# Performance work log

Hardware: AMD Instinct MI355X
Metric: run time of the kernel (lower is better)

## Reference

```python
import jax, jax.numpy as jnp
import numpy as np

N_HEADS = 16

def setup_inputs() -> dict:
    key = jax.random.key(0)
    ks = jax.random.split(key, 9)
    B, S, E = 2, 2048, 1024
    s = 1.0 / np.sqrt(E)
    return {
        "x":  jax.random.normal(ks[0], (B, S, E), jnp.float32),
        "Wq": jax.random.normal(ks[1], (E, E), jnp.float32) * s,
        "bq": jax.random.normal(ks[2], (E,), jnp.float32) * 0.01,
        "Wk": jax.random.normal(ks[3], (E, E), jnp.float32) * s,
        "bk": jax.random.normal(ks[4], (E,), jnp.float32) * 0.01,
        "Wv": jax.random.normal(ks[5], (E, E), jnp.float32) * s,
        "bv": jax.random.normal(ks[6], (E,), jnp.float32) * 0.01,
        "Wo": jax.random.normal(ks[7], (E, E), jnp.float32) * s,
        "bo": jax.random.normal(ks[8], (E,), jnp.float32) * 0.01,
    }

def reference(x, Wq, bq, Wk, bk, Wv, bv, Wo, bo):
    B, S, E = x.shape
    H = N_HEADS
    D = E // H
    # torch nn.Linear: y = x @ W.T + b
    q = (x @ Wq.T + bq).reshape(B, S, H, D)
    k = (x @ Wk.T + bk).reshape(B, S, H, D)
    v = (x @ Wv.T + bv).reshape(B, S, H, D)
    # scores: [B, H, Q, K]
    scores = jnp.einsum('bqnd,bknd->bnqk', q, k) / jnp.sqrt(jnp.float32(D))
    # NOTE: original code softmaxes over dim=1 == the HEADS axis (faithful quirk)
    attn = jax.nn.softmax(scores, axis=1)
    # dropout p=0 -> identity
    out = jnp.einsum('bnqk,bknd->bnqd', attn, v)      # [B, H, Q, D]
    out = out.transpose(0, 2, 1, 3).reshape(B, S, E)  # [B, S, E]
    return out @ Wo.T + bo
```

## Files before the change

kernel.cpp:

```cpp
#include <hip/hip_runtime.h>
#include <cstddef>
#include <cstdint>

#define BATCH 2
#define S_LEN 2048
#define E_DIM 1024
#define NH    16
#define HD    64
#define M_ROWS (BATCH * S_LEN)

#define QSCALE 0.18033688011112042f

typedef unsigned short u16;
typedef short     bf16x8 __attribute__((ext_vector_type(8)));
typedef _Float16  f16x8  __attribute__((ext_vector_type(8)));
typedef __fp16    h16x2  __attribute__((ext_vector_type(2)));
typedef float     f32x4  __attribute__((ext_vector_type(4)));

__device__ __forceinline__ u16 f2bf(float f) {
    union { float f; unsigned u; } v; v.f = f;
    unsigned r = v.u + 0x7fffu + ((v.u >> 16) & 1u);
    return (u16)(r >> 16);
}
__device__ __forceinline__ float bf2f(u16 h) {
    union { unsigned u; float f; } v; v.u = ((unsigned)h) << 16;
    return v.f;
}

__device__ __forceinline__ void load_lds16(const u16* g, u16* l) {
    __builtin_amdgcn_global_load_lds(
        (const __attribute__((address_space(1))) unsigned int*)g,
        (__attribute__((address_space(3))) unsigned int*)l, 16, 0, 0);
}

__global__ void cvt_bf16(const float* __restrict__ in, u16* __restrict__ out, int n)
{
    int i = (blockIdx.x * 256 + threadIdx.x) * 4;
    if (i + 3 < n) {
        float4 v = *(const float4*)(in + i);
        u16 o[4] = { f2bf(v.x), f2bf(v.y), f2bf(v.z), f2bf(v.w) };
        *(uint2*)(out + i) = *(const uint2*)o;
    }
}

__global__ void cvt_w3(const float* __restrict__ Wq, const float* __restrict__ Wk,
                       const float* __restrict__ Wv, u16* __restrict__ out)
{
    const int seg = blockIdx.y;
    const float* src = (seg == 0) ? Wq : (seg == 1) ? Wk : Wv;
    int i = (blockIdx.x * 256 + threadIdx.x) * 4;
    float4 v = *(const float4*)(src + i);
    u16 o[4] = { f2bf(v.x), f2bf(v.y), f2bf(v.z), f2bf(v.w) };
    *(uint2*)(out + (size_t)seg * E_DIM * E_DIM + i) = *(const uint2*)o;
}

__global__ void combine_ctx(const u16* __restrict__ a, const u16* __restrict__ b,
                            u16* __restrict__ c, int n)
{
    int i = (blockIdx.x * 256 + threadIdx.x) * 4;
    if (i + 3 < n) {
        uint2 ua = *(const uint2*)(a + i);
        uint2 ub = *(const uint2*)(b + i);
        const u16* pa = (const u16*)&ua; const u16* pb = (const u16*)&ub;
        u16 o[4];
#pragma unroll
        for (int j = 0; j < 4; ++j) o[j] = f2bf(bf2f(pa[j]) + bf2f(pb[j]));
        *(uint2*)(c + i) = *(const uint2*)o;
    }
}

__global__ __launch_bounds__(256)
void gemm_qkv(const u16* __restrict__ A, const u16* __restrict__ W3,
              const float* __restrict__ bq, const float* __restrict__ bk,
              const float* __restrict__ bv,
              u16* __restrict__ Qb, u16* __restrict__ Kb, u16* __restrict__ Vtb)
{
    __shared__ u16 Al[128 * 32];
    __shared__ u16 Bl[128 * 32];
    const int K = E_DIM;
    const int t = threadIdx.x;
    const int w = t >> 6, lane = t & 63;
    const int quad = lane >> 4, lm = lane & 15;
    const int wy = w >> 1, wx = w & 1;
    const int m0 = blockIdx.x * 128, n0 = blockIdx.y * 128;
    const int lrow  = lane >> 2;
    const int lcol8 = (lane & 3) * 8;

    f32x4 acc[4][4] = {};

    for (int kb = 0; kb < K; kb += 32) {
        __syncthreads();
#pragma unroll
        for (int i = 0; i < 2; ++i) {
            const int r0 = w * 32 + i * 16;
            load_lds16(A  + (size_t)(m0 + r0 + lrow) * K + kb + lcol8, &Al[r0 * 32]);
            load_lds16(W3 + (size_t)(n0 + r0 + lrow) * K + kb + lcol8, &Bl[r0 * 32]);
        }
        __syncthreads();

        bf16x8 af[4], bfr[4];
#pragma unroll
        for (int i = 0; i < 4; ++i)
            af[i] = *(const bf16x8*)(Al + (wy * 64 + i * 16 + lm) * 32 + quad * 8);
#pragma unroll
        for (int j = 0; j < 4; ++j)
            bfr[j] = *(const bf16x8*)(Bl + (wx * 64 + j * 16 + lm) * 32 + quad * 8);
#pragma unroll
        for (int i = 0; i < 4; ++i)
#pragma unroll
            for (int j = 0; j < 4; ++j)
                acc[i][j] = __builtin_amdgcn_mfma_f32_16x16x32_bf16(af[i], bfr[j], acc[i][j], 0, 0, 0);
    }

    const int seg = n0 >> 10;
    const int nl0 = n0 & 1023;
    const float* bs = (seg == 0) ? bq : (seg == 1) ? bk : bv;

    if (seg < 2) {
        u16* dst = (seg == 0) ? Qb : Kb;
        const float scl = (seg == 0) ? QSCALE : 1.0f;
#pragma unroll
        for (int j = 0; j < 4; ++j) {
            const int n = nl0 + wx * 64 + j * 16 + lm;
            const float bias = bs[n];
#pragma unroll
            for (int i = 0; i < 4; ++i) {
                const int mrow = m0 + wy * 64 + i * 16 + quad * 4;
#pragma unroll
                for (int rg = 0; rg < 4; ++rg)
                    dst[(size_t)(mrow + rg) * E_DIM + n] = f2bf((acc[i][j][rg] + bias) * scl);
            }
        }
    } else {
#pragma unroll
        for (int j = 0; j < 4; ++j) {
            const int n = nl0 + wx * 64 + j * 16 + lm;
            const float bias = bs[n];
#pragma unroll
            for (int i = 0; i < 4; ++i) {
                const int mrow = m0 + wy * 64 + i * 16 + quad * 4;
                const int batch = mrow >> 11;
                const int sloc  = mrow & 2047;
                u16 o[4];
#pragma unroll
                for (int rg = 0; rg < 4; ++rg) {
                    union { _Float16 h; u16 u; } cv;
                    cv.h = (_Float16)(acc[i][j][rg] + bias);
                    o[rg] = cv.u;
                }
                *(uint2*)&Vtb[(size_t)batch * E_DIM * S_LEN + (size_t)n * S_LEN + sloc]
                    = *(const uint2*)o;
            }
        }
    }
}

__global__ __launch_bounds__(256)
void gemm_wo(const u16* __restrict__ A, const u16* __restrict__ B,
             const float* __restrict__ bias, float* __restrict__ C)
{
    __shared__ u16 Al[128 * 32];
    __shared__ u16 Bl[128 * 32];
    const int K = E_DIM, N = E_DIM;
    const int t = threadIdx.x;
    const int w = t >> 6, lane = t & 63;
    const int quad = lane >> 4, lm = lane & 15;
    const int wy = w >> 1, wx = w & 1;
    const int m0 = blockIdx.x * 128, n0 = blockIdx.y * 128;
    const int lrow  = lane >> 2;
    const int lcol8 = (lane & 3) * 8;

    f32x4 acc[4][4] = {};

    for (int kb = 0; kb < K; kb += 32) {
        __syncthreads();
#pragma unroll
        for (int i = 0; i < 2; ++i) {
            const int r0 = w * 32 + i * 16;
            load_lds16(A + (size_t)(m0 + r0 + lrow) * K + kb + lcol8, &Al[r0 * 32]);
            load_lds16(B + (size_t)(n0 + r0 + lrow) * K + kb + lcol8, &Bl[r0 * 32]);
        }
        __syncthreads();

        bf16x8 af[4], bfr[4];
#pragma unroll
        for (int i = 0; i < 4; ++i)
            af[i] = *(const bf16x8*)(Al + (wy * 64 + i * 16 + lm) * 32 + quad * 8);
#pragma unroll
        for (int j = 0; j < 4; ++j)
            bfr[j] = *(const bf16x8*)(Bl + (wx * 64 + j * 16 + lm) * 32 + quad * 8);
#pragma unroll
        for (int i = 0; i < 4; ++i)
#pragma unroll
            for (int j = 0; j < 4; ++j)
                acc[i][j] = __builtin_amdgcn_mfma_f32_16x16x32_bf16(af[i], bfr[j], acc[i][j], 0, 0, 0);
    }

#pragma unroll
    for (int j = 0; j < 4; ++j) {
        const int n = n0 + wx * 64 + j * 16 + lm;
        const float bs = bias[n];
#pragma unroll
        for (int i = 0; i < 4; ++i) {
            const int mrow = m0 + wy * 64 + i * 16 + quad * 4;
#pragma unroll
            for (int rg = 0; rg < 4; ++rg)
                C[(size_t)(mrow + rg) * N + n] = acc[i][j][rg] + bs;
        }
    }
}

#define QKT_ST(S4W, KOFF)                                                     \
  _Pragma("unroll")                                                           \
  for (int kt = 0; kt < 2; ++kt) {                                            \
    f32x4 sacc_[2][2];                                                        \
    _Pragma("unroll")                                                         \
    for (int hp = 0; hp < 2; ++hp) {                                          \
      bf16x8 kf0_ = *(const bf16x8*)(K + kmat                                 \
                    + (size_t)((KOFF) + kt * 16 + lm) * E_DIM                 \
                    + (h0 + hp) * 64 + quad * 8);                             \
      bf16x8 kf1_ = *(const bf16x8*)(K + kmat                                 \
                    + (size_t)((KOFF) + kt * 16 + lm) * E_DIM                 \
                    + (h0 + hp) * 64 + 32 + quad * 8);                        \
      _Pragma("unroll")                                                       \
      for (int s = 0; s < 2; ++s) {                                           \
        f32x4 sf_ = {};                                                       \
        sf_ = __builtin_amdgcn_mfma_f32_16x16x32_bf16(kf0_, qf[s][hp][0], sf_, 0, 0, 0); \
        sf_ = __builtin_amdgcn_mfma_f32_16x16x32_bf16(kf1_, qf[s][hp][1], sf_, 0, 0, 0); \
        sacc_[hp][s] = sf_;                                                   \
      }                                                                       \
    }                                                                         \
    _Pragma("unroll")                                                         \
    for (int s = 0; s < 2; ++s)                                               \
      _Pragma("unroll")                                                       \
      for (int rg = 0; rg < 4; ++rg) {                                        \
        union { h16x2 v; unsigned u; } pk_;                                   \
        pk_.v = __builtin_amdgcn_cvt_pkrtz(sacc_[0][s][rg], sacc_[1][s][rg]); \
        const int kl_  = kt * 16 + quad * 4 + rg;                             \
        const int qph_ = ((s * 16 + lm) + 8 * quad) & 31;                     \
        *(unsigned*)((S4W) + (size_t)(kl_ * 32 + qph_) * 18 + 2 * w) = pk_.u; \
      }                                                                       \
  }

#define SM_ST(S4R, P5W)                                                       \
  {                                                                           \
    float pv0[16], pv1[16];                                                   \
    _Pragma("unroll")                                                         \
    for (int e = 0; e < 2; ++e) {                                             \
      const int kk_ = 2 * sj + e;                                             \
      const u16* base_ = (S4R) + (size_t)(kk_ * 32 + qrot) * 18;              \
      union { uint4 u; __fp16 hh[8]; } r0_, r1_;                              \
      r0_.u = *(const uint4*)(base_);                                         \
      r1_.u = *(const uint4*)(base_ + 8);                                     \
      float s_[16];                                                           \
      _Pragma("unroll")                                                       \
      for (int z = 0; z < 8; ++z) {                                           \
        s_[z] = (float)r0_.hh[z]; s_[8 + z] = (float)r1_.hh[z];               \
      }                                                                       \
      const float m_ =                                                        \
          fmaxf(fmaxf(fmaxf(fmaxf(s_[0], s_[1]), fmaxf(s_[2], s_[3])),        \
                      fmaxf(fmaxf(s_[4], s_[5]), fmaxf(s_[6], s_[7]))),       \
                fmaxf(fmaxf(fmaxf(s_[8], s_[9]), fmaxf(s_[10], s_[11])),      \
                      fmaxf(fmaxf(s_[12], s_[13]), fmaxf(s_[14], s_[15])))); \
      _Pragma("unroll")                                                       \
      for (int hh = 0; hh < 16; ++hh)                                         \
        s_[hh] = __builtin_amdgcn_exp2f(s_[hh] - m_);                         \
      const float sum_ =                                                      \
          (((s_[0] + s_[1]) + (s_[2] + s_[3])) + ((s_[4] + s_[5]) + (s_[6] + s_[7]))) + \
          (((s_[8] + s_[9]) + (s_[10] + s_[11])) + ((s_[12] + s_[13]) + (s_[14] + s_[15]))); \
      const float inv_ = __builtin_amdgcn_rcpf(sum_);                         \
      if (e == 0) {                                                           \
        _Pragma("unroll")                                                     \
        for (int hh = 0; hh < 16; ++hh) pv0[hh] = s_[hh] * inv_;              \
      } else {                                                                \
        _Pragma("unroll")                                                     \
        for (int hh = 0; hh < 16; ++hh) pv1[hh] = s_[hh] * inv_;              \
      }                                                                       \
    }                                                                         \
    _Pragma("unroll")                                                         \
    for (int hh = 0; hh < 16; ++hh) {                                         \
      union { h16x2 v; unsigned u; } cv_;                                     \
      cv_.v = __builtin_amdgcn_cvt_pkrtz(pv0[hh], pv1[hh]);                   \
      *(unsigned*)((P5W) + (size_t)hh * 1280 + sq * 40 + 2 * sj) = cv_.u;     \
    }                                                                         \
  }

#define V_ST(KOFF)                                                            \
  _Pragma("unroll")                                                           \
  for (int hp = 0; hp < 2; ++hp)                                              \
    _Pragma("unroll")                                                         \
    for (int dt = 0; dt < 4; ++dt)                                            \
      vf[hp][dt] = *(const f16x8*)(Vt + vtb                                   \
                   + (size_t)((h0 + hp) * 64 + dt * 16 + lm) * S_LEN          \
                   + (KOFF) + quad * 8);

#define PV_ST(P5R)                                                            \
  _Pragma("unroll")                                                           \
  for (int hp = 0; hp < 2; ++hp)                                              \
    _Pragma("unroll")                                                         \
    for (int s = 0; s < 2; ++s) {                                             \
      f16x8 pa_ = *(const f16x8*)((P5R) + (size_t)(h0 + hp) * 1280            \
                                  + (s * 16 + lm) * 40 + quad * 8);           \
      _Pragma("unroll")                                                       \
      for (int dt = 0; dt < 4; ++dt)                                          \
        oacc[hp][s][dt] = __builtin_amdgcn_mfma_f32_16x16x32_f16(             \
                              pa_, vf[hp][dt], oacc[hp][s][dt], 0, 0, 0);     \
    }

#define PHASE_END                                                             \
  asm volatile("s_waitcnt lgkmcnt(0)" ::: "memory");                          \
  __builtin_amdgcn_s_barrier();

__global__ __launch_bounds__(512, 2)
void attn_v16(const u16* __restrict__ Q, const u16* __restrict__ K,
              const u16* __restrict__ Vt, u16* __restrict__ ctxA,
              u16* __restrict__ ctxB)
{
    __shared__ __align__(16) u16 smem[77824];

    const int t     = threadIdx.x;
    const int w     = t >> 6;
    const int lane  = t & 63;
    const int quad  = lane >> 4, lm = lane & 15;

    const int i     = blockIdx.x;
    const int xcd   = i & 7;
    const int combo = xcd >> 1;
    const int b     = combo >> 1;
    const int khalf = combo & 1;
    const int slot  = i >> 3;
    const int qt    = ((xcd & 1) << 5) | slot;
    const int q0    = qt * 32;

    const size_t qbase = ((size_t)b * S_LEN + q0) * E_DIM;
    const size_t kmat  = (size_t)b * S_LEN * E_DIM;
    const size_t vtb   = (size_t)b * E_DIM * S_LEN;

    const int h0 = 2 * w;

    bf16x8 qf[2][2][2];
#pragma unroll
    for (int s = 0; s < 2; ++s)
#pragma unroll
        for (int hp = 0; hp < 2; ++hp)
#pragma unroll
            for (int hf = 0; hf < 2; ++hf)
                qf[s][hp][hf] = *(const bf16x8*)(Q + qbase
                                + (size_t)(s * 16 + lm) * E_DIM
                                + (h0 + hp) * 64 + hf * 32 + quad * 8);

    f32x4 oacc[2][2][4] = {};
    f16x8 vf[2][4];
    const int kbeg = khalf * (S_LEN / 2);
    const int sq = t & 31, sj = t >> 5;
    const int qrot = (sq + 8 * ((sj >> 1) & 3)) & 31;

    u16* const S4_0 = smem;
    u16* const S4_1 = smem + 18432;
    u16* const P5_0 = smem + 36864;
    u16* const P5_1 = smem + 57344;

    QKT_ST(S4_0, kbeg)
    PHASE_END
    QKT_ST(S4_1, kbeg + 32)
    SM_ST (S4_0, P5_0)
    PHASE_END

    for (int c = 2; c < 32; ++c) {
        u16* S4w = (c & 1) ? S4_1 : S4_0;
        u16* S4r = (c & 1) ? S4_0 : S4_1;
        u16* P5w = (c & 1) ? P5_0 : P5_1;
        u16* P5r = (c & 1) ? P5_1 : P5_0;
        V_ST  (kbeg + (c - 2) * 32)
        QKT_ST(S4w, kbeg + c * 32)
        SM_ST (S4r, P5w)
        PV_ST (P5r)
        PHASE_END
    }

    V_ST  (kbeg + 30 * 32)
    SM_ST (S4_1, P5_1)
    PV_ST (P5_0)
    PHASE_END
    V_ST  (kbeg + 31 * 32)
    PV_ST (P5_1)

    __syncthreads();
    u16* Ol = smem;
#pragma unroll
    for (int hp = 0; hp < 2; ++hp) {
        const int h = h0 + hp;
#pragma unroll
        for (int s = 0; s < 2; ++s)
#pragma unroll
            for (int dt = 0; dt < 4; ++dt)
#pragma unroll
                for (int rg = 0; rg < 4; ++rg)
                    Ol[(size_t)(s * 16 + quad * 4 + rg) * 1024 + h * 64 + dt * 16 + lm]
                        = f2bf(oacc[hp][s][dt][rg]);
    }
    __syncthreads();
    u16* dst = khalf ? ctxB : ctxA;
#pragma unroll
    for (int i2 = 0; i2 < 8; ++i2) {
        const int unit = i2 * 512 + t;
        const int r = unit >> 7, cu = unit & 127;
        *(bf16x8*)(dst + ((size_t)b * S_LEN + q0 + r) * E_DIM + cu * 8) =
            *(const bf16x8*)(Ol + (size_t)r * 1024 + cu * 8);
    }
}

#undef QKT_ST
#undef SM_ST
#undef V_ST
#undef PV_ST
#undef PHASE_END

extern "C" void kernel_launch(void* const* d_in, const int* in_sizes, int n_in,
                              void* d_out, int out_size, void* d_ws, size_t ws_size,
                              hipStream_t stream)
{
    const float* x  = (const float*)d_in[0];
    const float* Wq = (const float*)d_in[1];
    const float* bq = (const float*)d_in[2];
    const float* Wk = (const float*)d_in[3];
    const float* bk = (const float*)d_in[4];
    const float* Wv = (const float*)d_in[5];
    const float* bv = (const float*)d_in[6];
    const float* Wo = (const float*)d_in[7];
    const float* bo = (const float*)d_in[8];
    float* out = (float*)d_out;

    const size_t MAT = (size_t)M_ROWS * E_DIM;
    const size_t WSZ = (size_t)E_DIM * E_DIM;
    u16* xb   = (u16*)d_ws;
    u16* W3   = xb   + MAT;
    u16* Wob  = W3   + 3 * WSZ;
    u16* Qb   = Wob  + WSZ;
    u16* Kb   = Qb   + MAT;
    u16* Vtb  = Kb   + MAT;
    u16* ctxA = Vtb  + MAT;
    u16* ctxB = ctxA + MAT;

    cvt_bf16<<<(int)(MAT / 1024), 256, 0, stream>>>(x, xb, (int)MAT);
    dim3 wgrid(WSZ / 1024, 3);
    cvt_w3<<<wgrid, 256, 0, stream>>>(Wq, Wk, Wv, W3);
    cvt_bf16<<<(int)(WSZ / 1024), 256, 0, stream>>>(Wo, Wob, (int)WSZ);

    dim3 qkvgrid(M_ROWS / 128, 3 * E_DIM / 128);
    gemm_qkv<<<qkvgrid, 256, 0, stream>>>(xb, W3, bq, bk, bv, Qb, Kb, Vtb);

    attn_v16<<<BATCH * 64 * 2, 512, 0, stream>>>(Qb, Kb, Vtb, ctxA, ctxB);

    combine_ctx<<<(int)(MAT / 1024), 256, 0, stream>>>(ctxA, ctxB, xb, (int)MAT);

    dim3 ogrid(M_ROWS / 128, E_DIM / 128);
    gemm_wo<<<ogrid, 256, 0, stream>>>(xb, Wob, bo, out);
}
```

Before: 298.0 us.

## Double K-tile in GEMMs with XOR-swizzled LDS and register-prefetch K in attention

Both projection GEMMs now stage a 64-wide K slice per iteration instead of 32, halving the number of barrier pairs, and XOR-swizzle the LDS column groups so the fragment reads avoid bank conflicts. The attention kernel splits the K-fragment global loads out of the QK^T stage and loads the next chunk's K fragments into a second register set one phase ahead, with the main loop unrolled by two to ping-pong between them. This hides global load latency for K behind the softmax and PV work. The cost is doubled LDS per GEMM block and extra registers in the attention kernel, which runs under a launch bound of two blocks per unit and may spill.

```diff
diff --git a/kernel.cpp b/kernel.cpp
--- a/kernel.cpp
+++ b/kernel.cpp
@@ -75,41 +75,50 @@
               const float* __restrict__ bv,
               u16* __restrict__ Qb, u16* __restrict__ Kb, u16* __restrict__ Vtb)
 {
-    __shared__ u16 Al[128 * 32];
-    __shared__ u16 Bl[128 * 32];
+    __shared__ u16 Al[128 * 64];
+    __shared__ u16 Bl[128 * 64];
     const int K = E_DIM;
     const int t = threadIdx.x;
     const int w = t >> 6, lane = t & 63;
     const int quad = lane >> 4, lm = lane & 15;
     const int wy = w >> 1, wx = w & 1;
     const int m0 = blockIdx.x * 128, n0 = blockIdx.y * 128;
-    const int lrow  = lane >> 2;
-    const int lcol8 = (lane & 3) * 8;
+    const int lrow   = lane >> 3;
+    const int lcolsw = ((lane & 7) ^ lrow) * 8;
 
     f32x4 acc[4][4] = {};
 
-    for (int kb = 0; kb < K; kb += 32) {
+    for (int kb = 0; kb < K; kb += 64) {
         __syncthreads();
 #pragma unroll
-        for (int i = 0; i < 2; ++i) {
-            const int r0 = w * 32 + i * 16;
-            load_lds16(A  + (size_t)(m0 + r0 + lrow) * K + kb + lcol8, &Al[r0 * 32]);
-            load_lds16(W3 + (size_t)(n0 + r0 + lrow) * K + kb + lcol8, &Bl[r0 * 32]);
+        for (int i = 0; i < 4; ++i) {
+            const int r0 = w * 32 + i * 8;
+            load_lds16(A  + (size_t)(m0 + r0 + lrow) * K + kb + lcolsw, &Al[r0 * 64]);
+            load_lds16(W3 + (size_t)(n0 + r0 + lrow) * K + kb + lcolsw, &Bl[r0 * 64]);
         }
         __syncthreads();
 
-        bf16x8 af[4], bfr[4];
-#pragma unroll
-        for (int i = 0; i < 4; ++i)
-            af[i] = *(const bf16x8*)(Al + (wy * 64 + i * 16 + lm) * 32 + quad * 8);
-#pragma unroll
-        for (int j = 0; j < 4; ++j)
-            bfr[j] = *(const bf16x8*)(Bl + (wx * 64 + j * 16 + lm) * 32 + quad * 8);
-#pragma unroll
-        for (int i = 0; i < 4; ++i)
-#pragma unroll
-            for (int j = 0; j < 4; ++j)
-                acc[i][j] = __builtin_amdgcn_mfma_f32_16x16x32_bf16(af[i], bfr[j], acc[i][j], 0, 0, 0);
+#pragma unroll
+        for (int kk = 0; kk < 2; ++kk) {
+            bf16x8 af[4], bfr[4];
+#pragma unroll
+            for (int i = 0; i < 4; ++i) {
+                const int rr = wy * 64 + i * 16 + lm;
+                const int pg = (kk * 4 + quad) ^ (rr & 7);
+                af[i] = *(const bf16x8*)(Al + rr * 64 + pg * 8);
+            }
+#pragma unroll
+            for (int j = 0; j < 4; ++j) {
+                const int rr = wx * 64 + j * 16 + lm;
+                const int pg = (kk * 4 + quad) ^ (rr & 7);
+                bfr[j] = *(const bf16x8*)(Bl + rr * 64 + pg * 8);
+            }
+#pragma unroll
+            for (int i = 0; i < 4; ++i)
+#pragma unroll
+                for (int j = 0; j < 4; ++j)
+                    acc[i][j] = __builtin_amdgcn_mfma_f32_16x16x32_bf16(af[i], bfr[j], acc[i][j], 0, 0, 0);
+        }
     }
 
     const int seg = n0 >> 10;
@@ -159,41 +168,50 @@
 void gemm_wo(const u16* __restrict__ A, const u16* __restrict__ B,
              const float* __restrict__ bias, float* __restrict__ C)
 {
-    __shared__ u16 Al[128 * 32];
-    __shared__ u16 Bl[128 * 32];
+    __shared__ u16 Al[128 * 64];
+    __shared__ u16 Bl[128 * 64];
     const int K = E_DIM, N = E_DIM;
     const int t = threadIdx.x;
     const int w = t >> 6, lane = t & 63;
     const int quad = lane >> 4, lm = lane & 15;
     const int wy = w >> 1, wx = w & 1;
     const int m0 = blockIdx.x * 128, n0 = blockIdx.y * 128;
-    const int lrow  = lane >> 2;
-    const int lcol8 = (lane & 3) * 8;
+    const int lrow   = lane >> 3;
+    const int lcolsw = ((lane & 7) ^ lrow) * 8;
 
     f32x4 acc[4][4] = {};
 
-    for (int kb = 0; kb < K; kb += 32) {
+    for (int kb = 0; kb < K; kb += 64) {
         __syncthreads();
 #pragma unroll
-        for (int i = 0; i < 2; ++i) {
-            const int r0 = w * 32 + i * 16;
-            load_lds16(A + (size_t)(m0 + r0 + lrow) * K + kb + lcol8, &Al[r0 * 32]);
-            load_lds16(B + (size_t)(n0 + r0 + lrow) * K + kb + lcol8, &Bl[r0 * 32]);
+        for (int i = 0; i < 4; ++i) {
+            const int r0 = w * 32 + i * 8;
+            load_lds16(A + (size_t)(m0 + r0 + lrow) * K + kb + lcolsw, &Al[r0 * 64]);
+            load_lds16(B + (size_t)(n0 + r0 + lrow) * K + kb + lcolsw, &Bl[r0 * 64]);
         }
         __syncthreads();
 
-        bf16x8 af[4], bfr[4];
-#pragma unroll
-        for (int i = 0; i < 4; ++i)
-            af[i] = *(const bf16x8*)(Al + (wy * 64 + i * 16 + lm) * 32 + quad * 8);
-#pragma unroll
-        for (int j = 0; j < 4; ++j)
-            bfr[j] = *(const bf16x8*)(Bl + (wx * 64 + j * 16 + lm) * 32 + quad * 8);
-#pragma unroll
-        for (int i = 0; i < 4; ++i)
-#pragma unroll
-            for (int j = 0; j < 4; ++j)
-                acc[i][j] = __builtin_amdgcn_mfma_f32_16x16x32_bf16(af[i], bfr[j], acc[i][j], 0, 0, 0);
+#pragma unroll
+        for (int kk = 0; kk < 2; ++kk) {
+            bf16x8 af[4], bfr[4];
+#pragma unroll
+            for (int i = 0; i < 4; ++i) {
+                const int rr = wy * 64 + i * 16 + lm;
+                const int pg = (kk * 4 + quad) ^ (rr & 7);
+                af[i] = *(const bf16x8*)(Al + rr * 64 + pg * 8);
+            }
+#pragma unroll
+            for (int j = 0; j < 4; ++j) {
+                const int rr = wx * 64 + j * 16 + lm;
+                const int pg = (kk * 4 + quad) ^ (rr & 7);
+                bfr[j] = *(const bf16x8*)(Bl + rr * 64 + pg * 8);
+            }
+#pragma unroll
+            for (int i = 0; i < 4; ++i)
+#pragma unroll
+                for (int j = 0; j < 4; ++j)
+                    acc[i][j] = __builtin_amdgcn_mfma_f32_16x16x32_bf16(af[i], bfr[j], acc[i][j], 0, 0, 0);
+        }
     }
 
 #pragma unroll
@@ -210,26 +228,32 @@
     }
 }
 
-#define QKT_ST(S4W, KOFF)                                                     \
+#define KLOAD(KX, KOFF)                                                       \
+  _Pragma("unroll")                                                           \
+  for (int kt = 0; kt < 2; ++kt)                                              \
+    _Pragma("unroll")                                                         \
+    for (int hp = 0; hp < 2; ++hp) {                                          \
+      KX[kt][hp][0] = *(const bf16x8*)(K + kmat                               \
+                      + (size_t)((KOFF) + kt * 16 + lm) * E_DIM               \
+                      + (h0 + hp) * 64 + quad * 8);                           \
+      KX[kt][hp][1] = *(const bf16x8*)(K + kmat                               \
+                      + (size_t)((KOFF) + kt * 16 + lm) * E_DIM               \
+                      + (h0 + hp) * 64 + 32 + quad * 8);                      \
+    }
+
+#define QKT_R(KX, S4W)                                                        \
   _Pragma("unroll")                                                           \
   for (int kt = 0; kt < 2; ++kt) {                                            \
     f32x4 sacc_[2][2];                                                        \
     _Pragma("unroll")                                                         \
-    for (int hp = 0; hp < 2; ++hp) {                                          \
-      bf16x8 kf0_ = *(const bf16x8*)(K + kmat                                 \
-                    + (size_t)((KOFF) + kt * 16 + lm) * E_DIM                 \
-                    + (h0 + hp) * 64 + quad * 8);                             \
-      bf16x8 kf1_ = *(const bf16x8*)(K + kmat                                 \
-                    + (size_t)((KOFF) + kt * 16 + lm) * E_DIM                 \
-                    + (h0 + hp) * 64 + 32 + quad * 8);                        \
+    for (int hp = 0; hp < 2; ++hp)                                            \
       _Pragma("unroll")                                                       \
       for (int s = 0; s < 2; ++s) {                                           \
         f32x4 sf_ = {};                                                       \
-        sf_ = __builtin_amdgcn_mfma_f32_16x16x32_bf16(kf0_, qf[s][hp][0], sf_, 0, 0, 0); \
-        sf_ = __builtin_amdgcn_mfma_f32_16x16x32_bf16(kf1_, qf[s][hp][1], sf_, 0, 0, 0); \
+        sf_ = __builtin_amdgcn_mfma_f32_16x16x32_bf16(KX[kt][hp][0], qf[s][hp][0], sf_, 0, 0, 0); \
+        sf_ = __builtin_amdgcn_mfma_f32_16x16x32_bf16(KX[kt][hp][1], qf[s][hp][1], sf_, 0, 0, 0); \
         sacc_[hp][s] = sf_;                                                   \
       }                                                                       \
-    }                                                                         \
     _Pragma("unroll")                                                         \
     for (int s = 0; s < 2; ++s)                                               \
       _Pragma("unroll")                                                       \
@@ -312,7 +336,7 @@
   __builtin_amdgcn_s_barrier();
 
 __global__ __launch_bounds__(512, 2)
-void attn_v16(const u16* __restrict__ Q, const u16* __restrict__ K,
+void attn_v17(const u16* __restrict__ Q, const u16* __restrict__ K,
               const u16* __restrict__ Vt, u16* __restrict__ ctxA,
               u16* __restrict__ ctxB)
 {
@@ -351,6 +375,7 @@
 
     f32x4 oacc[2][2][4] = {};
     f16x8 vf[2][4];
+    bf16x8 kA[2][2][2], kB[2][2][2];
     const int kbeg = khalf * (S_LEN / 2);
     const int sq = t & 31, sj = t >> 5;
     const int qrot = (sq + 8 * ((sj >> 1) & 3)) & 31;
@@ -360,21 +385,29 @@
     u16* const P5_0 = smem + 36864;
     u16* const P5_1 = smem + 57344;
 
-    QKT_ST(S4_0, kbeg)
+    KLOAD(kA, kbeg)
+    QKT_R (kA, S4_0)
+    KLOAD (kB, kbeg + 32)
     PHASE_END
-    QKT_ST(S4_1, kbeg + 32)
+    QKT_R (kB, S4_1)
+    KLOAD (kA, kbeg + 64)
     SM_ST (S4_0, P5_0)
     PHASE_END
 
-    for (int c = 2; c < 32; ++c) {
-        u16* S4w = (c & 1) ? S4_1 : S4_0;
-        u16* S4r = (c & 1) ? S4_0 : S4_1;
-        u16* P5w = (c & 1) ? P5_0 : P5_1;
-        u16* P5r = (c & 1) ? P5_1 : P5_0;
-        V_ST  (kbeg + (c - 2) * 32)
-        QKT_ST(S4w, kbeg + c * 32)
-        SM_ST (S4r, P5w)
-        PV_ST (P5r)
+    for (int it = 0; it < 15; ++it) {
+        const int c0 = 2 + 2 * it;
+        V_ST  (kbeg + (c0 - 2) * 32)
+        QKT_R (kA, S4_0)
+        KLOAD (kB, kbeg + (c0 + 1) * 32)
+        SM_ST (S4_1, P5_1)
+        PV_ST (P5_0)
+        PHASE_END
+        const int nk = (c0 + 2 < 32) ? (c0 + 2) : 31;
+        V_ST  (kbeg + (c0 - 1) * 32)
+        QKT_R (kB, S4_1)
+        KLOAD (kA, kbeg + nk * 32)
+        SM_ST (S4_0, P5_0)
+        PV_ST (P5_1)
         PHASE_END
     }
 
@@ -410,7 +443,8 @@
     }
 }
 
-#undef QKT_ST
+#undef KLOAD
+#undef QKT_R
 #undef SM_ST
 #undef V_ST
 #undef PV_ST
@@ -450,7 +484,7 @@
     dim3 qkvgrid(M_ROWS / 128, 3 * E_DIM / 128);
     gemm_qkv<<<qkvgrid, 256, 0, stream>>>(xb, W3, bq, bk, bv, Qb, Kb, Vtb);
 
-    attn_v16<<<BATCH * 64 * 2, 512, 0, stream>>>(Qb, Kb, Vtb, ctxA, ctxB);
+    attn_v17<<<BATCH * 64 * 2, 512, 0, stream>>>(Qb, Kb, Vtb, ctxA, ctxB);
 
     combine_ctx<<<(int)(MAT / 1024), 256, 0, stream>>>(ctxA, ctxB, xb, (int)MAT);
 
```

Result: no change. 303.1 us (+1.7%).
